# Optimization experiments

Hardware: AMD Instinct MI355X
Metric: run time of the kernel (lower is better)

The kernel has to match this reference:

```python
import jax, jax.numpy as jnp
import numpy as np

DIM = 1024
N_HEADS = 16
HEAD_DIM = DIM // N_HEADS
EPS = 1e-05
ROPE_BASE = 1000000.0


def apply_rope(x, base=ROPE_BASE):
    # x: [b, seq, heads, head_dim]
    b, seq, n_heads, dim = x.shape
    half = dim // 2
    i = jnp.arange(half)
    theta = 1.0 / base ** (2 * i / dim)
    pos = jnp.arange(seq)
    angles = pos[:, None] * theta[None, :]            # [seq, half]
    cos = jnp.cos(angles)[None, :, None, :]           # [1, seq, 1, half]
    sin = jnp.sin(angles)[None, :, None, :]
    x1, x2 = jnp.split(x, 2, axis=-1)
    return jnp.concatenate([x1 * cos - x2 * sin, x1 * sin + x2 * cos], axis=-1)


def setup_inputs() -> dict:
    key = jax.random.key(0)
    ks = jax.random.split(key, 6)
    b, seq = 2, 2048
    scale = 1.0 / np.sqrt(DIM)
    x = jax.random.normal(ks[0], (b, seq, DIM), dtype=jnp.float32)
    w_norm = jnp.ones((DIM,), dtype=jnp.float32)
    Wq = jax.random.normal(ks[1], (DIM, DIM), dtype=jnp.float32) * scale
    Wk = jax.random.normal(ks[2], (DIM, DIM), dtype=jnp.float32) * scale
    Wv = jax.random.normal(ks[3], (DIM, DIM), dtype=jnp.float32) * scale
    Wo = jax.random.normal(ks[4], (DIM, DIM), dtype=jnp.float32) * scale
    return {"x": x, "w_norm": w_norm, "Wq": Wq, "Wk": Wk, "Wv": Wv, "Wo": Wo}


def reference(x, w_norm, Wq, Wk, Wv, Wo):
    b, seq, d = x.shape
    # RMSNorm
    rms = jnp.sqrt(jnp.mean(x * x, axis=-1, keepdims=True) + EPS)
    x_norm = x / rms * w_norm
    # QKV projections (Dense without bias: y = x @ W)
    q = (x_norm @ Wq).reshape(b, seq, N_HEADS, HEAD_DIM)
    k = (x_norm @ Wk).reshape(b, seq, N_HEADS, HEAD_DIM)
    v = (x_norm @ Wv).reshape(b, seq, N_HEADS, HEAD_DIM)
    q = apply_rope(q)
    k = apply_rope(k)
    # Causal attention with full [b,h,t,s] scores (faithful to source)
    scores = jnp.einsum('bthd,bshd->bhts', q, k) / jnp.sqrt(jnp.float32(HEAD_DIM))
    causal = jnp.triu(jnp.full((seq, seq), -jnp.inf, dtype=scores.dtype), k=1)
    scores = scores + causal[None, None, :, :]
    attn = jax.nn.softmax(scores, axis=-1)
    out = jnp.einsum('bhts,bshd->bthd', attn, v).reshape(b, seq, d)
    return out @ Wo
```

## Files before the change

### kernel.cpp

```cpp
#include <hip/hip_runtime.h>

#define DIM 1024
#define SEQ 2048
#define BATCH 2
#define NHEADS 16
#define HD 64
#define ROWS (BATCH * SEQ)

typedef __bf16 bf16x8 __attribute__((ext_vector_type(8)));
typedef __bf16 bf16x4 __attribute__((ext_vector_type(4)));
typedef float f32x4 __attribute__((ext_vector_type(4)));
typedef float f32x16 __attribute__((ext_vector_type(16)));
typedef unsigned u32x4 __attribute__((ext_vector_type(4)));

__device__ __forceinline__ f32x4 f4zero() {
    f32x4 z = {0.f, 0.f, 0.f, 0.f};
    return z;
}

__device__ __forceinline__ unsigned cvtpk(float lo, float hi) {
    unsigned r;
    asm("v_cvt_pk_bf16_f32 %0, %1, %2" : "=v"(r) : "v"(lo), "v"(hi));
    return r;
}

__device__ __forceinline__ void pl32swap(unsigned& a, unsigned& b) {
    asm volatile("v_permlane32_swap_b32 %0, %1" : "+v"(a), "+v"(b));
}

#define GLOAD_LDS16(g, l)                                                                  \
    __builtin_amdgcn_global_load_lds((const __attribute__((address_space(1))) void*)(g),   \
                                     (__attribute__((address_space(3))) void*)(l), 16, 0, 0)

__global__ __launch_bounds__(256) void rmsnorm_bf16(const float* __restrict__ x,
                                                    const float* __restrict__ w,
                                                    __bf16* __restrict__ xn) {
    int row = blockIdx.x;
    int t = threadIdx.x;
    float4 v = ((const float4*)(x + (size_t)row * DIM))[t];
    float ss = v.x * v.x + v.y * v.y + v.z * v.z + v.w * v.w;
#pragma unroll
    for (int off = 1; off < 64; off <<= 1) ss += __shfl_xor(ss, off);
    __shared__ float red[4];
    if ((t & 63) == 0) red[t >> 6] = ss;
    __syncthreads();
    ss = red[0] + red[1] + red[2] + red[3];
    float scale = rsqrtf(ss * (1.0f / DIM) + 1e-5f);
    float4 wv = ((const float4*)w)[t];
    bf16x4 o;
    o[0] = (__bf16)(v.x * scale * wv.x);
    o[1] = (__bf16)(v.y * scale * wv.y);
    o[2] = (__bf16)(v.z * scale * wv.z);
    o[3] = (__bf16)(v.w * scale * wv.w);
    *(bf16x4*)(xn + (size_t)row * DIM + t * 4) = o;
}

__global__ __launch_bounds__(256) void wcvt_kernel(const float* __restrict__ Wq,
                                                   const float* __restrict__ Wk,
                                                   const float* __restrict__ Wv,
                                                   const float* __restrict__ Wo,
                                                   __bf16* tq, __bf16* tk, __bf16* tv, __bf16* to_) {
    int z = blockIdx.z;
    const float* W = z == 0 ? Wq : z == 1 ? Wk : z == 2 ? Wv : Wo;
    __bf16* T = z == 0 ? tq : z == 1 ? tk : z == 2 ? tv : to_;
    __shared__ float tile[32][33];
    int n0 = blockIdx.x * 32, k0 = blockIdx.y * 32;
    int tx = threadIdx.x & 31, ty = threadIdx.x >> 5;
#pragma unroll
    for (int j = 0; j < 32; j += 8) tile[ty + j][tx] = W[(size_t)(k0 + ty + j) * DIM + n0 + tx];
    __syncthreads();
#pragma unroll
    for (int j = 0; j < 32; j += 8)
        T[(size_t)(n0 + ty + j) * DIM + k0 + tx] = (__bf16)tile[tx][ty + j];
}

__global__ __launch_bounds__(256) void rope_table_kernel(float* __restrict__ cosT,
                                                         float* __restrict__ sinT) {
    int idx = blockIdx.x * 256 + threadIdx.x;
    int s = idx >> 5, i = idx & 31;
    float e = (2.0f * (float)i) / 64.0f;
    float theta = 1.0f / powf(1000000.0f, e);
    float ang = (float)s * theta;
    cosT[idx] = cosf(ang);
    sinT[idx] = sinf(ang);
}

__device__ __forceinline__ void gemm_core(const __bf16* __restrict__ A,
                                          const __bf16* __restrict__ Bt,
                                          int K, __bf16* As, __bf16* Bs,
                                          f32x4 (&acc)[4][4], int row0, int col0) {
    int tid = threadIdx.x;
    int w = tid >> 6, l = tid & 63, l15 = l & 15, g = l >> 4;
    int wr = (w >> 1) << 6, wc = (w & 1) << 6;

    int sr0 = tid >> 2;
    int sr1 = 64 + (tid >> 2);
    int lc0 = (((tid & 3) ^ ((tid >> 3) & 3)) << 3);
    const __bf16* gA0 = A + (size_t)(row0 + sr0) * K + lc0;
    const __bf16* gA1 = A + (size_t)(row0 + sr1) * K + lc0;
    const __bf16* gB0 = Bt + (size_t)(col0 + sr0) * K + lc0;
    const __bf16* gB1 = Bt + (size_t)(col0 + sr1) * K + lc0;
    __bf16* lA0 = As + w * 512;
    __bf16* lA1 = As + 2048 + w * 512;
    __bf16* lB0 = Bs + w * 512;
    __bf16* lB1 = Bs + 2048 + w * 512;

    int rca = ((g ^ ((l15 >> 1) & 3)) << 3);

#pragma unroll
    for (int i = 0; i < 4; ++i)
#pragma unroll
        for (int j = 0; j < 4; ++j) acc[i][j] = f4zero();

    for (int k0 = 0; k0 < K; k0 += 32) {
        __syncthreads();
        GLOAD_LDS16(gA0 + k0, lA0);
        GLOAD_LDS16(gA1 + k0, lA1);
        GLOAD_LDS16(gB0 + k0, lB0);
        GLOAD_LDS16(gB1 + k0, lB1);
        __syncthreads();

        bf16x8 af[4], bfr[4];
#pragma unroll
        for (int i = 0; i < 4; ++i) af[i] = *(const bf16x8*)&As[(wr + i * 16 + l15) * 32 + rca];
#pragma unroll
        for (int j = 0; j < 4; ++j) bfr[j] = *(const bf16x8*)&Bs[(wc + j * 16 + l15) * 32 + rca];
        __builtin_amdgcn_s_setprio(1);
#pragma unroll
        for (int i = 0; i < 4; ++i)
#pragma unroll
            for (int j = 0; j < 4; ++j)
                acc[i][j] = __builtin_amdgcn_mfma_f32_16x16x32_bf16(af[i], bfr[j], acc[i][j], 0, 0, 0);
        __builtin_amdgcn_s_setprio(0);
    }
}

__global__ __launch_bounds__(256) void gemm_qkv_kernel(const __bf16* __restrict__ xn,
                                                       const __bf16* __restrict__ wq,
                                                       const __bf16* __restrict__ wk,
                                                       const __bf16* __restrict__ wv,
                                                       __bf16* __restrict__ qo,
                                                       __bf16* __restrict__ ko,
                                                       __bf16* __restrict__ vt,
                                                       const float* __restrict__ cosT,
                                                       const float* __restrict__ sinT) {
    __shared__ __bf16 As[128 * 32];
    __shared__ __bf16 Bs[128 * 32];
    int z = blockIdx.z;
    const __bf16* Bt = z == 0 ? wq : z == 1 ? wk : wv;
    int row0 = (int)blockIdx.y << 7, col0 = (int)blockIdx.x << 7;
    f32x4 acc[4][4];
    gemm_core(xn, Bt, DIM, As, Bs, acc, row0, col0);

    int tid = threadIdx.x;
    int w = tid >> 6, l = tid & 63, l15 = l & 15, g = l >> 4;
    int wr = (w >> 1) << 6, wc = (w & 1) << 6;
    int colbase = col0 + wc;

    if (z == 2) {
        int bh = ((row0 >> 11) << 4) + (colbase >> 6);
#pragma unroll
        for (int i = 0; i < 4; ++i) {
            int sbase = (row0 + wr + i * 16 + g * 4) & (SEQ - 1);
#pragma unroll
            for (int j = 0; j < 4; ++j) {
                int d = j * 16 + l15;
                bf16x4 o;
#pragma unroll
                for (int r = 0; r < 4; ++r) o[r] = (__bf16)acc[i][j][r];
                *(bf16x4*)&vt[((size_t)bh * HD + d) * SEQ + sbase] = o;
            }
        }
    } else {
        __bf16* C = z == 0 ? qo : ko;
#pragma unroll
        for (int i = 0; i < 4; ++i) {
#pragma unroll
            for (int r = 0; r < 4; ++r) {
                int row = row0 + wr + i * 16 + g * 4 + r;
                int s = row & (SEQ - 1);
#pragma unroll
                for (int j = 0; j < 2; ++j) {
                    float c = cosT[s * 32 + j * 16 + l15];
                    float sn = sinT[s * 32 + j * 16 + l15];
                    float x1 = acc[i][j][r], x2 = acc[i][j + 2][r];
                    C[(size_t)row * DIM + colbase + j * 16 + l15] = (__bf16)(x1 * c - x2 * sn);
                    C[(size_t)row * DIM + colbase + (j + 2) * 16 + l15] = (__bf16)(x1 * sn + x2 * c);
                }
            }
        }
    }
}

__global__ __launch_bounds__(256) void gemm_out_kernel(const __bf16* __restrict__ ctx,
                                                       const __bf16* __restrict__ wo,
                                                       float* __restrict__ out) {
    __shared__ __bf16 As[128 * 32];
    __shared__ __bf16 Bs[128 * 32];
    int row0 = (int)blockIdx.y << 7, col0 = (int)blockIdx.x << 7;
    f32x4 acc[4][4];
    gemm_core(ctx, wo, DIM, As, Bs, acc, row0, col0);
    int tid = threadIdx.x;
    int w = tid >> 6, l = tid & 63, l15 = l & 15, g = l >> 4;
    int wr = (w >> 1) << 6, wc = (w & 1) << 6;
#pragma unroll
    for (int i = 0; i < 4; ++i)
#pragma unroll
        for (int j = 0; j < 4; ++j)
#pragma unroll
            for (int r = 0; r < 4; ++r) {
                int row = row0 + wr + i * 16 + g * 4 + r;
                int col = col0 + wc + j * 16 + l15;
                out[(size_t)row * DIM + col] = acc[i][j][r];
            }
}

__global__ __launch_bounds__(256) void attn_mfma_kernel(const __bf16* __restrict__ q,
                                                        const __bf16* __restrict__ k,
                                                        const __bf16* __restrict__ vt,
                                                        __bf16* __restrict__ ctx) {
    int bh = blockIdx.x;
    int qb = 15 - (int)blockIdx.y;
    int b = bh >> 4, h = bh & 15;
    __shared__ __bf16 Ks[64][72];
    __shared__ __bf16 Vs[64][72];
    int tid = threadIdx.x, w = tid >> 6, l = tid & 63;
    int l31 = l & 31, hi = l >> 5;
    size_t hoff = (size_t)(b * SEQ) * DIM + h * HD;
    const __bf16* vth = vt + (size_t)bh * HD * SEQ;
    int qw0 = qb * 128 + w * 32;
    int qrow = qw0 + l31;
    int qmax = qw0 + 31;
    int nst = 2 * qb + 2;

    bf16x8 qf[4];
    const float c2 = 0.125f * 1.44269504f;
#pragma unroll
    for (int g = 0; g < 4; ++g) {
        bf16x8 t0 = *(const bf16x8*)&q[hoff + (size_t)qrow * DIM + g * 16 + hi * 8];
#pragma unroll
        for (int e = 0; e < 8; ++e) qf[g][e] = (__bf16)((float)t0[e] * c2);
    }

    f32x16 oA, oB;
#pragma unroll
    for (int r = 0; r < 16; ++r) {
        oA[r] = 0.f;
        oB[r] = 0.f;
    }
    float m_run = -1e30f, l_run = 0.f;

    int sr = tid >> 3, sc = (tid & 7) * 8;
    bf16x8 rk0, rk1, rv0, rv1;
    rk0 = *(const bf16x8*)&k[hoff + (size_t)sr * DIM + sc];
    rk1 = *(const bf16x8*)&k[hoff + (size_t)(32 + sr) * DIM + sc];
    rv0 = *(const bf16x8*)&vth[(size_t)sr * SEQ + sc];
    rv1 = *(const bf16x8*)&vth[(size_t)(32 + sr) * SEQ + sc];

    for (int st = 0; st < nst; ++st) {
        int s0 = st << 6;
        __syncthreads();
        *(bf16x8*)&Ks[sr][sc] = rk0;
        *(bf16x8*)&Ks[32 + sr][sc] = rk1;
        *(bf16x8*)&Vs[sr][sc] = rv0;
        *(bf16x8*)&Vs[32 + sr][sc] = rv1;
        __syncthreads();
        if (st + 1 < nst) {
            int sn = s0 + 64;
            rk0 = *(const bf16x8*)&k[hoff + (size_t)(sn + sr) * DIM + sc];
            rk1 = *(const bf16x8*)&k[hoff + (size_t)(sn + 32 + sr) * DIM + sc];
            rv0 = *(const bf16x8*)&vth[(size_t)sr * SEQ + sn + sc];
            rv1 = *(const bf16x8*)&vth[(size_t)(32 + sr) * SEQ + sn + sc];
        }
        if (s0 > qmax) continue;

        f32x16 sa, sb;
#pragma unroll
        for (int r = 0; r < 16; ++r) {
            sa[r] = 0.f;
            sb[r] = 0.f;
        }
        __builtin_amdgcn_s_setprio(1);
#pragma unroll
        for (int g = 0; g < 4; ++g) {
            bf16x8 ka = *(const bf16x8*)&Ks[l31][g * 16 + hi * 8];
            bf16x8 kb2 = *(const bf16x8*)&Ks[32 + l31][g * 16 + hi * 8];
            sa = __builtin_amdgcn_mfma_f32_32x32x16_bf16(ka, qf[g], sa, 0, 0, 0);
            sb = __builtin_amdgcn_mfma_f32_32x32x16_bf16(kb2, qf[g], sb, 0, 0, 0);
        }
        __builtin_amdgcn_s_setprio(0);

        if (s0 + 63 > qw0) {
#pragma unroll
            for (int r = 0; r < 16; ++r) {
                int kg = s0 + (r & 3) + 8 * (r >> 2) + 4 * hi;
                if (kg > qrow) sa[r] = -1e30f;
                if (kg + 32 > qrow) sb[r] = -1e30f;
            }
        }

        float lmax = -3e38f;
#pragma unroll
        for (int r = 0; r < 16; ++r) lmax = fmaxf(lmax, fmaxf(sa[r], sb[r]));
        if (!__all(lmax <= m_run + 10.0f)) {
            float omax = fmaxf(lmax, __shfl_xor(lmax, 32));
            float m_new = fmaxf(m_run, omax);
            float alpha = exp2f(m_run - m_new);
            l_run *= alpha;
#pragma unroll
            for (int r = 0; r < 16; ++r) {
                oA[r] *= alpha;
                oB[r] *= alpha;
            }
            m_run = m_new;
        }
        float ls = 0.f;
#pragma unroll
        for (int r = 0; r < 16; ++r) {
            sa[r] = exp2f(sa[r] - m_run);
            ls += sa[r];
            sb[r] = exp2f(sb[r] - m_run);
            ls += sb[r];
        }
        l_run += ls + __shfl_xor(ls, 32);

        bf16x8 pa[4];
#pragma unroll
        for (int g = 0; g < 2; ++g) {
            unsigned a_ = cvtpk(sa[8 * g + 0], sa[8 * g + 1]);
            unsigned b_ = cvtpk(sa[8 * g + 4], sa[8 * g + 5]);
            pl32swap(a_, b_);
            unsigned c_ = cvtpk(sa[8 * g + 2], sa[8 * g + 3]);
            unsigned d_ = cvtpk(sa[8 * g + 6], sa[8 * g + 7]);
            pl32swap(c_, d_);
            u32x4 t4 = {a_, c_, b_, d_};
            pa[g] = __builtin_bit_cast(bf16x8, t4);
        }
#pragma unroll
        for (int g = 0; g < 2; ++g) {
            unsigned a_ = cvtpk(sb[8 * g + 0], sb[8 * g + 1]);
            unsigned b_ = cvtpk(sb[8 * g + 4], sb[8 * g + 5]);
            pl32swap(a_, b_);
            unsigned c_ = cvtpk(sb[8 * g + 2], sb[8 * g + 3]);
            unsigned d_ = cvtpk(sb[8 * g + 6], sb[8 * g + 7]);
            pl32swap(c_, d_);
            u32x4 t4 = {a_, c_, b_, d_};
            pa[2 + g] = __builtin_bit_cast(bf16x8, t4);
        }

        __builtin_amdgcn_s_setprio(1);
#pragma unroll
        for (int ks = 0; ks < 4; ++ks) {
            bf16x8 va = *(const bf16x8*)&Vs[l31][ks * 16 + hi * 8];
            bf16x8 vb2 = *(const bf16x8*)&Vs[32 + l31][ks * 16 + hi * 8];
            oA = __builtin_amdgcn_mfma_f32_32x32x16_bf16(va, pa[ks], oA, 0, 0, 0);
            oB = __builtin_amdgcn_mfma_f32_32x32x16_bf16(vb2, pa[ks], oB, 0, 0, 0);
        }
        __builtin_amdgcn_s_setprio(0);
    }

    float inv = 1.0f / l_run;
#pragma unroll
    for (int r = 0; r < 16; r += 2) {
        int d = (r & 3) + 8 * (r >> 2) + 4 * hi;
        unsigned pA = cvtpk(oA[r] * inv, oA[r + 1] * inv);
        unsigned pB = cvtpk(oB[r] * inv, oB[r + 1] * inv);
        *(unsigned*)&ctx[hoff + (size_t)qrow * DIM + d] = pA;
        *(unsigned*)&ctx[hoff + (size_t)qrow * DIM + 32 + d] = pB;
    }
}

extern "C" void kernel_launch(void* const* d_in, const int* in_sizes, int n_in,
                              void* d_out, int out_size, void* d_ws, size_t ws_size,
                              hipStream_t stream) {
    const float* x = (const float*)d_in[0];
    const float* w_norm = (const float*)d_in[1];
    const float* Wq = (const float*)d_in[2];
    const float* Wk = (const float*)d_in[3];
    const float* Wv = (const float*)d_in[4];
    const float* Wo = (const float*)d_in[5];
    float* out = (float*)d_out;
    char* w8 = (char*)d_ws;

    __bf16* xn = (__bf16*)(w8);
    __bf16* wtq = (__bf16*)(w8 + (8ull << 20));
    __bf16* wtk = (__bf16*)(w8 + (10ull << 20));
    __bf16* wtv = (__bf16*)(w8 + (12ull << 20));
    __bf16* wto = (__bf16*)(w8 + (14ull << 20));
    __bf16* qb = (__bf16*)(w8 + (16ull << 20));
    __bf16* kb = (__bf16*)(w8 + (24ull << 20));
    __bf16* vtb = (__bf16*)(w8 + (32ull << 20));
    __bf16* ctx = (__bf16*)(w8 + (40ull << 20));
    float* cosT = (float*)(w8 + (48ull << 20));
    float* sinT = cosT + SEQ * 32;

    wcvt_kernel<<<dim3(32, 32, 4), 256, 0, stream>>>(Wq, Wk, Wv, Wo, wtq, wtk, wtv, wto);
    rmsnorm_bf16<<<ROWS, 256, 0, stream>>>(x, w_norm, xn);
    rope_table_kernel<<<(SEQ * 32) / 256, 256, 0, stream>>>(cosT, sinT);

    gemm_qkv_kernel<<<dim3(DIM / 128, ROWS / 128, 3), 256, 0, stream>>>(
        xn, wtq, wtk, wtv, qb, kb, vtb, cosT, sinT);

    attn_mfma_kernel<<<dim3(BATCH * NHEADS, SEQ / 128), 256, 0, stream>>>(qb, kb, vtb, ctx);

    gemm_out_kernel<<<dim3(DIM / 128, ROWS / 128), 256, 0, stream>>>(ctx, wto, out);
}
```

Baseline: 150.8 us.

## Compute V transposed via swapped GEMM and halve attention query tile

```diff
diff --git a/kernel.cpp b/kernel.cpp
--- a/kernel.cpp
+++ b/kernel.cpp
@@ -146,33 +146,18 @@
                                                        const float* __restrict__ sinT) {
     __shared__ __bf16 As[128 * 32];
     __shared__ __bf16 Bs[128 * 32];
-    int z = blockIdx.z;
-    const __bf16* Bt = z == 0 ? wq : z == 1 ? wk : wv;
-    int row0 = (int)blockIdx.y << 7, col0 = (int)blockIdx.x << 7;
-    f32x4 acc[4][4];
-    gemm_core(xn, Bt, DIM, As, Bs, acc, row0, col0);
-
+    int bid = blockIdx.x;
     int tid = threadIdx.x;
     int w = tid >> 6, l = tid & 63, l15 = l & 15, g = l >> 4;
     int wr = (w >> 1) << 6, wc = (w & 1) << 6;
-    int colbase = col0 + wc;
-
-    if (z == 2) {
-        int bh = ((row0 >> 11) << 4) + (colbase >> 6);
-#pragma unroll
-        for (int i = 0; i < 4; ++i) {
-            int sbase = (row0 + wr + i * 16 + g * 4) & (SEQ - 1);
-#pragma unroll
-            for (int j = 0; j < 4; ++j) {
-                int d = j * 16 + l15;
-                bf16x4 o;
-#pragma unroll
-                for (int r = 0; r < 4; ++r) o[r] = (__bf16)acc[i][j][r];
-                *(bf16x4*)&vt[((size_t)bh * HD + d) * SEQ + sbase] = o;
-            }
-        }
-    } else {
-        __bf16* C = z == 0 ? qo : ko;
+    f32x4 acc[4][4];
+
+    if (bid < 512) {
+        int z = bid >> 8, t = bid & 255;
+        int col0 = (t & 7) << 7, row0 = (t >> 3) << 7;
+        gemm_core(xn, z ? wk : wq, DIM, As, Bs, acc, row0, col0);
+        __bf16* C = z ? ko : qo;
+        int colbase = col0 + wc;
 #pragma unroll
         for (int i = 0; i < 4; ++i) {
 #pragma unroll
@@ -189,6 +174,23 @@
                 }
             }
         }
+    } else {
+        int t = bid - 512;
+        int b = t >> 7, r7 = t & 127;
+        int row0 = (r7 >> 4) << 7;
+        int col0 = (r7 & 15) << 7;
+        gemm_core(wv, xn + (size_t)b * SEQ * DIM, DIM, As, Bs, acc, row0, col0);
+        __bf16* C = vt + (size_t)b * (NHEADS * HD) * SEQ;
+#pragma unroll
+        for (int i = 0; i < 4; ++i)
+#pragma unroll
+            for (int j = 0; j < 4; ++j)
+#pragma unroll
+                for (int r = 0; r < 4; ++r) {
+                    int row = row0 + wr + i * 16 + g * 4 + r;
+                    int col = col0 + wc + j * 16 + l15;
+                    C[(size_t)row * SEQ + col] = (__bf16)acc[i][j][r];
+                }
     }
 }
 
@@ -215,12 +217,12 @@
             }
 }
 
-__global__ __launch_bounds__(256) void attn_mfma_kernel(const __bf16* __restrict__ q,
+__global__ __launch_bounds__(128) void attn_mfma_kernel(const __bf16* __restrict__ q,
                                                         const __bf16* __restrict__ k,
                                                         const __bf16* __restrict__ vt,
                                                         __bf16* __restrict__ ctx) {
     int bh = blockIdx.x;
-    int qb = 15 - (int)blockIdx.y;
+    int qb = 31 - (int)blockIdx.y;
     int b = bh >> 4, h = bh & 15;
     __shared__ __bf16 Ks[64][72];
     __shared__ __bf16 Vs[64][72];
@@ -228,10 +230,9 @@
     int l31 = l & 31, hi = l >> 5;
     size_t hoff = (size_t)(b * SEQ) * DIM + h * HD;
     const __bf16* vth = vt + (size_t)bh * HD * SEQ;
-    int qw0 = qb * 128 + w * 32;
+    int qw0 = qb * 64 + w * 32;
     int qrow = qw0 + l31;
-    int qmax = qw0 + 31;
-    int nst = 2 * qb + 2;
+    int nst = qb + 1;
 
     bf16x8 qf[4];
     const float c2 = 0.125f * 1.44269504f;
@@ -251,28 +252,30 @@
     float m_run = -1e30f, l_run = 0.f;
 
     int sr = tid >> 3, sc = (tid & 7) * 8;
-    bf16x8 rk0, rk1, rv0, rv1;
-    rk0 = *(const bf16x8*)&k[hoff + (size_t)sr * DIM + sc];
-    rk1 = *(const bf16x8*)&k[hoff + (size_t)(32 + sr) * DIM + sc];
-    rv0 = *(const bf16x8*)&vth[(size_t)sr * SEQ + sc];
-    rv1 = *(const bf16x8*)&vth[(size_t)(32 + sr) * SEQ + sc];
+    bf16x8 rk[4], rv[4];
+#pragma unroll
+    for (int c = 0; c < 4; ++c) {
+        rk[c] = *(const bf16x8*)&k[hoff + (size_t)(c * 16 + sr) * DIM + sc];
+        rv[c] = *(const bf16x8*)&vth[(size_t)(c * 16 + sr) * SEQ + sc];
+    }
 
     for (int st = 0; st < nst; ++st) {
         int s0 = st << 6;
         __syncthreads();
-        *(bf16x8*)&Ks[sr][sc] = rk0;
-        *(bf16x8*)&Ks[32 + sr][sc] = rk1;
-        *(bf16x8*)&Vs[sr][sc] = rv0;
-        *(bf16x8*)&Vs[32 + sr][sc] = rv1;
+#pragma unroll
+        for (int c = 0; c < 4; ++c) {
+            *(bf16x8*)&Ks[c * 16 + sr][sc] = rk[c];
+            *(bf16x8*)&Vs[c * 16 + sr][sc] = rv[c];
+        }
         __syncthreads();
         if (st + 1 < nst) {
             int sn = s0 + 64;
-            rk0 = *(const bf16x8*)&k[hoff + (size_t)(sn + sr) * DIM + sc];
-            rk1 = *(const bf16x8*)&k[hoff + (size_t)(sn + 32 + sr) * DIM + sc];
-            rv0 = *(const bf16x8*)&vth[(size_t)sr * SEQ + sn + sc];
-            rv1 = *(const bf16x8*)&vth[(size_t)(32 + sr) * SEQ + sn + sc];
-        }
-        if (s0 > qmax) continue;
+#pragma unroll
+            for (int c = 0; c < 4; ++c) {
+                rk[c] = *(const bf16x8*)&k[hoff + (size_t)(sn + c * 16 + sr) * DIM + sc];
+                rv[c] = *(const bf16x8*)&vth[(size_t)(c * 16 + sr) * SEQ + sn + sc];
+            }
+        }
 
         f32x16 sa, sb;
 #pragma unroll
@@ -361,12 +364,12 @@
 
     float inv = 1.0f / l_run;
 #pragma unroll
-    for (int r = 0; r < 16; r += 2) {
-        int d = (r & 3) + 8 * (r >> 2) + 4 * hi;
-        unsigned pA = cvtpk(oA[r] * inv, oA[r + 1] * inv);
-        unsigned pB = cvtpk(oB[r] * inv, oB[r + 1] * inv);
-        *(unsigned*)&ctx[hoff + (size_t)qrow * DIM + d] = pA;
-        *(unsigned*)&ctx[hoff + (size_t)qrow * DIM + 32 + d] = pB;
+    for (int rr = 0; rr < 16; rr += 4) {
+        int d = 8 * (rr >> 2) + 4 * hi;
+        uint2 pA = {cvtpk(oA[rr] * inv, oA[rr + 1] * inv), cvtpk(oA[rr + 2] * inv, oA[rr + 3] * inv)};
+        uint2 pB = {cvtpk(oB[rr] * inv, oB[rr + 1] * inv), cvtpk(oB[rr + 2] * inv, oB[rr + 3] * inv)};
+        *(uint2*)&ctx[hoff + (size_t)qrow * DIM + d] = pA;
+        *(uint2*)&ctx[hoff + (size_t)qrow * DIM + 32 + d] = pB;
     }
 }
 
@@ -398,10 +401,9 @@
     rmsnorm_bf16<<<ROWS, 256, 0, stream>>>(x, w_norm, xn);
     rope_table_kernel<<<(SEQ * 32) / 256, 256, 0, stream>>>(cosT, sinT);
 
-    gemm_qkv_kernel<<<dim3(DIM / 128, ROWS / 128, 3), 256, 0, stream>>>(
-        xn, wtq, wtk, wtv, qb, kb, vtb, cosT, sinT);
-
-    attn_mfma_kernel<<<dim3(BATCH * NHEADS, SEQ / 128), 256, 0, stream>>>(qb, kb, vtb, ctx);
+    gemm_qkv_kernel<<<768, 256, 0, stream>>>(xn, wtq, wtk, wtv, qb, kb, vtb, cosT, sinT);
+
+    attn_mfma_kernel<<<dim3(BATCH * NHEADS, SEQ / 64), 128, 0, stream>>>(qb, kb, vtb, ctx);
 
     gemm_out_kernel<<<dim3(DIM / 128, ROWS / 128), 256, 0, stream>>>(ctx, wto, out);
 }
```

Result: faster. 137.5 us (-8.8%).
